# Kernel tuning notes

Measured on AMD Instinct MI355X. Metric: run time of the kernel, lower is better.

The kernel has to match this reference:

```python
import jax, jax.numpy as jnp
import numpy as np

D_MODEL = 1024
NUM_HEADS = 16
D_K = D_MODEL // NUM_HEADS


def setup_inputs() -> dict:
    key = jax.random.key(0)
    ks = jax.random.split(key, 5)
    s = 1.0 / np.sqrt(D_MODEL)  # xavier-ish scale
    x = jax.random.normal(ks[0], (2, 2048, D_MODEL), dtype=jnp.float32)
    Wq = jax.random.normal(ks[1], (D_MODEL, D_MODEL), dtype=jnp.float32) * s
    Wk = jax.random.normal(ks[2], (D_MODEL, D_MODEL), dtype=jnp.float32) * s
    Wv = jax.random.normal(ks[3], (D_MODEL, D_MODEL), dtype=jnp.float32) * s
    Wo = jax.random.normal(ks[4], (D_MODEL, D_MODEL), dtype=jnp.float32) * s
    z = jnp.zeros((D_MODEL,), dtype=jnp.float32)
    return {"x": x, "Wq": Wq, "bq": z, "Wk": Wk, "bk": z, "Wv": Wv, "bv": z, "Wo": Wo, "bo": z}


def reference(x, Wq, bq, Wk, bk, Wv, bv, Wo, bo):
    B, S, _ = x.shape
    # torch Linear: y = x @ W.T + b
    def split_heads(t):
        return t.reshape(B, S, NUM_HEADS, D_K).transpose(0, 2, 1, 3)  # [B,H,S,Dk]
    q = split_heads(x @ Wq.T + bq)
    k = split_heads(x @ Wk.T + bk)
    v = split_heads(x @ Wv.T + bv)
    scores = jnp.einsum('bhqd,bhkd->bhqk', q, k) / jnp.sqrt(jnp.float32(D_K))
    attn = jax.nn.softmax(scores, axis=-1)
    out = jnp.einsum('bhqk,bhkd->bhqd', attn, v)  # [B,H,S,Dk]
    out = out.transpose(0, 2, 1, 3).reshape(B, S, D_MODEL)
    return out @ Wo.T + bo
```

## Files before the change

### kernel.cpp

```cpp
#include <hip/hip_runtime.h>
#include <hip/hip_bf16.h>
#include <type_traits>


typedef __attribute__((ext_vector_type(4))) float f32x4;
typedef __attribute__((ext_vector_type(16))) float f32x16;
typedef __attribute__((ext_vector_type(8))) short s16x8;
typedef __attribute__((ext_vector_type(4))) unsigned int u32x4;

#define GLDS16(g, l)                                                       \
  __builtin_amdgcn_global_load_lds(                                        \
      (const __attribute__((address_space(1))) unsigned int*)(g),          \
      (__attribute__((address_space(3))) unsigned int*)(l), 16, 0, 0)

#define SCALE_Q 0.18033688011112042f

__device__ __forceinline__ unsigned short f2bf(float f) {
  unsigned int u = __builtin_bit_cast(unsigned int, f);
  u += 0x7fffu + ((u >> 16) & 1u);
  return (unsigned short)(u >> 16);
}

__device__ __forceinline__ unsigned int cvtpk_bf16(float lo, float hi) {
  unsigned int r;
  asm("v_cvt_pk_bf16_f32 %0, %1, %2" : "=v"(r) : "v"(lo), "v"(hi));
  return r;
}

__device__ __forceinline__ float fexp2(float x) {
  return __builtin_amdgcn_exp2f(x);
}

__global__ void cvt_all(const float* __restrict__ x, const float* __restrict__ Wq,
                        const float* __restrict__ Wk, const float* __restrict__ Wv,
                        const float* __restrict__ Wo, const float* __restrict__ bq,
                        const float* __restrict__ bk, const float* __restrict__ bv,
                        unsigned short* __restrict__ xb,
                        unsigned short* __restrict__ wcat,
                        unsigned short* __restrict__ wob,
                        float* __restrict__ bcat) {
  int g = blockIdx.x * blockDim.x + threadIdx.x;
  if (g >= 2097152) {
    int off = (g - 2097152) * 4;
    const float* src;
    float sc = 1.0f;
    int o2 = off;
    if (off < 1024) {
      src = bq; sc = SCALE_Q;
    } else if (off < 2048) {
      src = bk; o2 = off - 1024;
    } else {
      src = bv; o2 = off - 2048;
    }
    float4 v = *reinterpret_cast<const float4*>(src + o2);
    float4 w;
    w.x = v.x * sc; w.y = v.y * sc; w.z = v.z * sc; w.w = v.w * sc;
    *reinterpret_cast<float4*>(bcat + off) = w;
    return;
  }
  const float* in;
  unsigned short* out;
  int off;
  float scale = 1.0f;
  if (g < 1048576) {
    in = x; out = xb; off = g;
  } else if (g < 1310720) {
    in = Wq; out = wcat; off = g - 1048576; scale = SCALE_Q;
  } else if (g < 1572864) {
    in = Wk; out = wcat + 1048576; off = g - 1310720;
  } else if (g < 1835008) {
    in = Wv; out = wcat + 2097152; off = g - 1572864;
  } else {
    in = Wo; out = wob; off = g - 1835008;
  }
  float4 v = *reinterpret_cast<const float4*>(in + off * 4);
  ushort4 o;
  o.x = f2bf(v.x * scale); o.y = f2bf(v.y * scale);
  o.z = f2bf(v.z * scale); o.w = f2bf(v.w * scale);
  *reinterpret_cast<ushort4*>(out + off * 4) = o;
}

__global__ __launch_bounds__(256, 3) void gemm_qkv(
    const unsigned short* __restrict__ A, const unsigned short* __restrict__ B,
    unsigned short* __restrict__ C, unsigned short* __restrict__ vtp,
    const float* __restrict__ bias) {
  __shared__ __align__(16) unsigned short As[3 * 128 * 32];
  __shared__ __align__(16) unsigned short Bs[3 * 128 * 32];

  const int tid = threadIdx.x;
  const int lane = tid & 63, wv = tid >> 6;
  const int g = lane >> 4, c16 = lane & 15;
  const int wm = wv >> 1, wn = wv & 1;
  const int bn = blockIdx.x, bm = blockIdx.y;

  const unsigned short* Ab = A + (size_t)(bm * 128) * 1024;
  const unsigned short* Bb = B + (size_t)(bn * 128) * 1024;

  const int r0 = tid >> 2, cc0 = (tid & 3) * 8;
  const int r1 = r0 + 64;
  const int cs0 = cc0 ^ ((r0 & 8) << 1);
  const int cs1 = cc0 ^ ((r1 & 8) << 1);
  const int rc = (g * 8) ^ ((c16 & 8) << 1);

  f32x4 acc[4][4] = {};

#define STG(mat, base, kt, slot)                                           \
  {                                                                        \
    GLDS16(base + (size_t)r0 * 1024 + (kt) * 32 + cs0,                     \
           mat + (slot) * 4096 + r0 * 32 + cc0);                           \
    GLDS16(base + (size_t)r1 * 1024 + (kt) * 32 + cs1,                     \
           mat + (slot) * 4096 + r1 * 32 + cc0);                           \
  }

  STG(As, Ab, 0, 0)
  STG(Bs, Bb, 0, 0)
  STG(As, Ab, 1, 1)
  STG(Bs, Bb, 1, 1)

  int slot = 0, slot2 = 2;
  for (int t = 0; t < 32; ++t) {
    if (t < 31) {
      asm volatile("s_waitcnt vmcnt(4)" ::: "memory");
    } else {
      asm volatile("s_waitcnt vmcnt(0)" ::: "memory");
    }
    __builtin_amdgcn_s_barrier();
    if (t < 30) {
      STG(As, Ab, t + 2, slot2)
      STG(Bs, Bb, t + 2, slot2)
    }
    s16x8 af[4], bf[4];
#pragma unroll
    for (int mf = 0; mf < 4; ++mf)
      af[mf] = *(const s16x8*)&As[slot * 4096 +
                                  (wm * 64 + mf * 16 + c16) * 32 + rc];
#pragma unroll
    for (int nf = 0; nf < 4; ++nf)
      bf[nf] = *(const s16x8*)&Bs[slot * 4096 +
                                  (wn * 64 + nf * 16 + c16) * 32 + rc];
    __builtin_amdgcn_s_setprio(1);
#pragma unroll
    for (int mf = 0; mf < 4; ++mf)
#pragma unroll
      for (int nf = 0; nf < 4; ++nf)
        acc[mf][nf] = __builtin_amdgcn_mfma_f32_16x16x32_bf16(
            af[mf], bf[nf], acc[mf][nf], 0, 0, 0);
    __builtin_amdgcn_s_setprio(0);
    slot = (slot == 2) ? 0 : slot + 1;
    slot2 = (slot2 == 2) ? 0 : slot2 + 1;
  }
#undef STG

#pragma unroll
  for (int mf = 0; mf < 4; ++mf) {
#pragma unroll
    for (int nf = 0; nf < 4; ++nf) {
      int col = bn * 128 + wn * 64 + nf * 16 + c16;
      float bb = bias[col];
      int row0 = bm * 128 + wm * 64 + mf * 16 + g * 4;
      if (col >= 2048) {
        int d = col - 2048, hh = d >> 6, dl = d & 63;
        int b_ = row0 >> 11, s = row0 & 2047;
        ushort4 pk;
        pk.x = f2bf(acc[mf][nf][0] + bb);
        pk.y = f2bf(acc[mf][nf][1] + bb);
        pk.z = f2bf(acc[mf][nf][2] + bb);
        pk.w = f2bf(acc[mf][nf][3] + bb);
        *reinterpret_cast<ushort4*>(
            vtp + ((size_t)((b_ * 16 + hh) * 64 + dl)) * 2048 + s) = pk;
      } else {
#pragma unroll
        for (int j = 0; j < 4; ++j)
          C[(size_t)(row0 + j) * 3072 + col] = f2bf(acc[mf][nf][j] + bb);
      }
    }
  }
}

__global__ __launch_bounds__(256, 4) void gemm_out64(
    const unsigned short* __restrict__ A, const unsigned short* __restrict__ B,
    float* __restrict__ C, const float* __restrict__ bias) {
  __shared__ __align__(16) unsigned short As[3 * 128 * 32];
  __shared__ __align__(16) unsigned short Bs[3 * 64 * 32];

  const int tid = threadIdx.x;
  const int lane = tid & 63, wv = tid >> 6;
  const int g = lane >> 4, c16 = lane & 15;
  const int wm = wv >> 1, wn = wv & 1;
  const int bn = blockIdx.x, bm = blockIdx.y;

  const unsigned short* Ab = A + (size_t)(bm * 128) * 1024;
  const unsigned short* Bb = B + (size_t)(bn * 64) * 1024;

  const int r0 = tid >> 2, cc0 = (tid & 3) * 8;
  const int r1 = r0 + 64;
  const int cs0 = cc0 ^ ((r0 & 8) << 1);
  const int cs1 = cc0 ^ ((r1 & 8) << 1);
  const int rc = (g * 8) ^ ((c16 & 8) << 1);

  f32x4 acc[4][2] = {};

#define STG64(kt, slot)                                                    \
  {                                                                        \
    GLDS16(Ab + (size_t)r0 * 1024 + (kt) * 32 + cs0,                       \
           As + (slot) * 4096 + r0 * 32 + cc0);                            \
    GLDS16(Ab + (size_t)r1 * 1024 + (kt) * 32 + cs1,                       \
           As + (slot) * 4096 + r1 * 32 + cc0);                            \
    GLDS16(Bb + (size_t)r0 * 1024 + (kt) * 32 + cs0,                       \
           Bs + (slot) * 2048 + r0 * 32 + cc0);                            \
  }

  STG64(0, 0)
  STG64(1, 1)

  int slot = 0, slot2 = 2;
  for (int t = 0; t < 32; ++t) {
    if (t < 31) {
      asm volatile("s_waitcnt vmcnt(3)" ::: "memory");
    } else {
      asm volatile("s_waitcnt vmcnt(0)" ::: "memory");
    }
    __builtin_amdgcn_s_barrier();
    if (t < 30) STG64(t + 2, slot2)
    s16x8 af[4], bf[2];
#pragma unroll
    for (int mf = 0; mf < 4; ++mf)
      af[mf] = *(const s16x8*)&As[slot * 4096 +
                                  (wm * 64 + mf * 16 + c16) * 32 + rc];
#pragma unroll
    for (int nf = 0; nf < 2; ++nf)
      bf[nf] = *(const s16x8*)&Bs[slot * 2048 +
                                  (wn * 32 + nf * 16 + c16) * 32 + rc];
    __builtin_amdgcn_s_setprio(1);
#pragma unroll
    for (int mf = 0; mf < 4; ++mf)
#pragma unroll
      for (int nf = 0; nf < 2; ++nf)
        acc[mf][nf] = __builtin_amdgcn_mfma_f32_16x16x32_bf16(
            af[mf], bf[nf], acc[mf][nf], 0, 0, 0);
    __builtin_amdgcn_s_setprio(0);
    slot = (slot == 2) ? 0 : slot + 1;
    slot2 = (slot2 == 2) ? 0 : slot2 + 1;
  }
#undef STG64

#pragma unroll
  for (int mf = 0; mf < 4; ++mf) {
#pragma unroll
    for (int nf = 0; nf < 2; ++nf) {
      int col = bn * 64 + wn * 32 + nf * 16 + c16;
      float bb = bias[col];
      int row0 = bm * 128 + wm * 64 + mf * 16 + g * 4;
#pragma unroll
      for (int j = 0; j < 4; ++j)
        C[(size_t)(row0 + j) * 1024 + col] = acc[mf][nf][j] + bb;
    }
  }
}

__global__ __launch_bounds__(1024) void flash_attn(
    const unsigned short* __restrict__ qkv, const unsigned short* __restrict__ vt,
    unsigned short* __restrict__ attn) {
  __shared__ __align__(16) char smem[131072];
  unsigned short* KsB = (unsigned short*)smem;
  unsigned short* VTsB = (unsigned short*)(smem + 65536);
  float* MoB = (float*)smem;
  float* MlB = (float*)(smem + 66560);

  const int tid = threadIdx.x;
  const int wv = tid >> 6, lane = tid & 63;
  const int half = wv >> 3, w8 = wv & 7;
  const int col = lane & 31, hi = lane >> 5;
  const int bh = blockIdx.x, qt = blockIdx.y;
  const int b = bh >> 4, h = bh & 15;
  const int qrow0 = qt * 256 + w8 * 32;

  const int stid = tid & 511;
  const int srow = stid >> 3, scs = stid & 7;
  const int sqc = ((scs - (srow >> 3)) & 7) ^ (srow & 7);
  const int kbase = half * 1024;
  const unsigned short* kgsrc =
      qkv + (size_t)(b * 2048 + kbase + srow) * 3072 + 1024 + h * 64 + sqc * 8;
  const unsigned short* vgsrc =
      vt + (size_t)(bh * 64 + srow) * 2048 + kbase + sqc * 8;

  s16x8 qb[4];
#pragma unroll
  for (int ds = 0; ds < 4; ++ds)
    qb[ds] = *(const s16x8*)(qkv + (size_t)(b * 2048 + qrow0 + col) * 3072 +
                             h * 64 + ds * 16 + hi * 8);

  s16x8 onev;
#pragma unroll
  for (int j = 0; j < 8; ++j) onev[j] = (short)0x3F80;

  f32x16 o[2] = {};
  f32x16 lacc = {};

  GLDS16(kgsrc, &KsB[(half * 4 + 0) * 4096 + stid * 8]);
  GLDS16(vgsrc, &VTsB[(half * 4 + 0) * 4096 + stid * 8]);
  GLDS16(kgsrc + (size_t)64 * 3072, &KsB[(half * 4 + 1) * 4096 + stid * 8]);
  GLDS16(vgsrc + 64, &VTsB[(half * 4 + 1) * 4096 + stid * 8]);

  for (int kt = 0; kt < 16; ++kt) {
    const int buf = kt & 3;
    const unsigned short* Kc = &KsB[(half * 4 + buf) * 4096];
    const unsigned short* Vc = &VTsB[(half * 4 + buf) * 4096];
    if (kt < 14) {
      const int nb = (kt + 2) & 3;
      GLDS16(kgsrc + (size_t)(kt + 2) * 64 * 3072,
             &KsB[(half * 4 + nb) * 4096 + stid * 8]);
      GLDS16(vgsrc + (kt + 2) * 64, &VTsB[(half * 4 + nb) * 4096 + stid * 8]);
      asm volatile("s_waitcnt vmcnt(4)" ::: "memory");
    } else if (kt == 14) {
      asm volatile("s_waitcnt vmcnt(2)" ::: "memory");
    } else {
      asm volatile("s_waitcnt vmcnt(0)" ::: "memory");
    }
    __builtin_amdgcn_s_barrier();

    f32x16 st[2];
    __builtin_amdgcn_s_setprio(1);
#pragma unroll
    for (int kb = 0; kb < 2; ++kb) {
      f32x16 a = {};
#pragma unroll
      for (int ds = 0; ds < 4; ++ds) {
        int row = kb * 32 + col;
        int cs = ds * 2 + hi;
        int hoff = ((cs ^ (row & 7)) + (row >> 3)) & 7;
        s16x8 ka = *(const s16x8*)&Kc[row * 64 + hoff * 8];
        a = __builtin_amdgcn_mfma_f32_32x32x16_bf16(ka, qb[ds], a, 0, 0, 0);
      }
      st[kb] = a;
    }
    __builtin_amdgcn_s_setprio(0);

#pragma unroll
    for (int kb = 0; kb < 2; ++kb)
#pragma unroll
      for (int r = 0; r < 16; ++r) st[kb][r] = fexp2(st[kb][r]);

#pragma unroll
    for (int kb = 0; kb < 2; ++kb) {
#pragma unroll
      for (int hf = 0; hf < 2; ++hf) {
        const int p0 = hf * 8;
        unsigned int a0 = cvtpk_bf16(st[kb][p0 + 0], st[kb][p0 + 1]);
        unsigned int b0 = cvtpk_bf16(st[kb][p0 + 4], st[kb][p0 + 5]);
        unsigned int a1 = cvtpk_bf16(st[kb][p0 + 2], st[kb][p0 + 3]);
        unsigned int b1 = cvtpk_bf16(st[kb][p0 + 6], st[kb][p0 + 7]);
        asm("v_permlane32_swap_b32 %0, %1" : "+v"(a0), "+v"(b0));
        asm("v_permlane32_swap_b32 %0, %1" : "+v"(a1), "+v"(b1));
        u32x4 pw;
        pw[0] = a0; pw[1] = a1; pw[2] = b0; pw[3] = b1;
        const s16x8 pa = __builtin_bit_cast(s16x8, pw);
        const int ks = kb * 2 + hf;
        __builtin_amdgcn_s_setprio(1);
#pragma unroll
        for (int n = 0; n < 2; ++n) {
          int row = n * 32 + col;
          int cs = ks * 2 + hi;
          int hoff = ((cs ^ (row & 7)) + (row >> 3)) & 7;
          s16x8 vb = *(const s16x8*)&Vc[row * 64 + hoff * 8];
          o[n] = __builtin_amdgcn_mfma_f32_32x32x16_bf16(pa, vb, o[n], 0, 0, 0);
        }
        lacc = __builtin_amdgcn_mfma_f32_32x32x16_bf16(pa, onev, lacc, 0, 0, 0);
        __builtin_amdgcn_s_setprio(0);
      }
    }
  }
  __syncthreads();

  if (half == 1) {
#pragma unroll
    for (int r = 0; r < 16; ++r) {
      int qd = (r & 3) + 8 * (r >> 2) + 4 * hi;
      MoB[(w8 * 32 + qd) * 65 + col] = o[0][r];
      MoB[(w8 * 32 + qd) * 65 + 32 + col] = o[1][r];
      if (col == 0) MlB[w8 * 32 + qd] = lacc[r];
    }
  }
  __syncthreads();
  if (half == 0) {
#pragma unroll
    for (int r = 0; r < 16; ++r) {
      int qd = (r & 3) + 8 * (r >> 2) + 4 * hi;
      float linv = 1.f / (lacc[r] + MlB[w8 * 32 + qd]);
      float v0 = (o[0][r] + MoB[(w8 * 32 + qd) * 65 + col]) * linv;
      float v1 = (o[1][r] + MoB[(w8 * 32 + qd) * 65 + 32 + col]) * linv;
      size_t base = (size_t)(b * 2048 + qrow0 + qd) * 1024 + h * 64;
      attn[base + col] = f2bf(v0);
      attn[base + 32 + col] = f2bf(v1);
    }
  }
}

extern "C" void kernel_launch(void* const* d_in, const int* in_sizes, int n_in,
                              void* d_out, int out_size, void* d_ws, size_t ws_size,
                              hipStream_t stream) {
  const float* x  = (const float*)d_in[0];
  const float* Wq = (const float*)d_in[1];
  const float* bq = (const float*)d_in[2];
  const float* Wk = (const float*)d_in[3];
  const float* bk = (const float*)d_in[4];
  const float* Wv = (const float*)d_in[5];
  const float* bv = (const float*)d_in[6];
  const float* Wo = (const float*)d_in[7];
  const float* bo = (const float*)d_in[8];
  float* out = (float*)d_out;

  char* ws = (char*)d_ws;
  const size_t MB = 1024 * 1024;
  unsigned short* xb   = (unsigned short*)(ws + 0);
  unsigned short* attn = (unsigned short*)(ws + 0);
  unsigned short* wob  = (unsigned short*)(ws + 8 * MB);
  unsigned short* wcat = (unsigned short*)(ws + 10 * MB);
  unsigned short* qkv  = (unsigned short*)(ws + 18 * MB);
  unsigned short* vt   = (unsigned short*)(ws + 42 * MB);
  float* bcat          = (float*)(ws + 50 * MB);

  cvt_all<<<8195, 256, 0, stream>>>(x, Wq, Wk, Wv, Wo, bq, bk, bv, xb, wcat,
                                    wob, bcat);

  gemm_qkv<<<dim3(24, 32), 256, 0, stream>>>(xb, wcat, qkv, vt, bcat);

  flash_attn<<<dim3(32, 8), 1024, 0, stream>>>(qkv, vt, attn);

  gemm_out64<<<dim3(16, 32), 256, 0, stream>>>(attn, wob, out, bo);
}
```

Baseline: 108.4 us.

## Process two 32-row query groups per wave in flash attention, halving block threads

```diff
diff --git a/kernel.cpp b/kernel.cpp
--- a/kernel.cpp
+++ b/kernel.cpp
@@ -258,7 +258,7 @@
   }
 }
 
-__global__ __launch_bounds__(1024) void flash_attn(
+__global__ __launch_bounds__(512) void flash_attn(
     const unsigned short* __restrict__ qkv, const unsigned short* __restrict__ vt,
     unsigned short* __restrict__ attn) {
   __shared__ __align__(16) char smem[131072];
@@ -269,92 +269,114 @@
 
   const int tid = threadIdx.x;
   const int wv = tid >> 6, lane = tid & 63;
-  const int half = wv >> 3, w8 = wv & 7;
+  const int half = wv >> 2, w4 = wv & 3;
   const int col = lane & 31, hi = lane >> 5;
   const int bh = blockIdx.x, qt = blockIdx.y;
   const int b = bh >> 4, h = bh & 15;
-  const int qrow0 = qt * 256 + w8 * 32;
-
-  const int stid = tid & 511;
-  const int srow = stid >> 3, scs = stid & 7;
-  const int sqc = ((scs - (srow >> 3)) & 7) ^ (srow & 7);
+  const int qrow0 = qt * 256 + w4 * 64;
+
+  const int stid = tid & 255;
+  const int idx0 = stid, idx1 = stid + 256;
+  const int sr0 = idx0 >> 3, sq0 = (((idx0 & 7) - (sr0 >> 3)) & 7) ^ (sr0 & 7);
+  const int sr1 = idx1 >> 3, sq1 = (((idx1 & 7) - (sr1 >> 3)) & 7) ^ (sr1 & 7);
   const int kbase = half * 1024;
-  const unsigned short* kgsrc =
-      qkv + (size_t)(b * 2048 + kbase + srow) * 3072 + 1024 + h * 64 + sqc * 8;
-  const unsigned short* vgsrc =
-      vt + (size_t)(bh * 64 + srow) * 2048 + kbase + sqc * 8;
-
-  s16x8 qb[4];
-#pragma unroll
-  for (int ds = 0; ds < 4; ++ds)
-    qb[ds] = *(const s16x8*)(qkv + (size_t)(b * 2048 + qrow0 + col) * 3072 +
-                             h * 64 + ds * 16 + hi * 8);
+  const unsigned short* kg0 =
+      qkv + (size_t)(b * 2048 + kbase + sr0) * 3072 + 1024 + h * 64 + sq0 * 8;
+  const unsigned short* kg1 =
+      qkv + (size_t)(b * 2048 + kbase + sr1) * 3072 + 1024 + h * 64 + sq1 * 8;
+  const unsigned short* vg0 =
+      vt + (size_t)(bh * 64 + sr0) * 2048 + kbase + sq0 * 8;
+  const unsigned short* vg1 =
+      vt + (size_t)(bh * 64 + sr1) * 2048 + kbase + sq1 * 8;
+
+#define STGF(kt, bf)                                                       \
+  {                                                                        \
+    unsigned short* kd = &KsB[(half * 4 + (bf)) * 4096];                   \
+    unsigned short* vd = &VTsB[(half * 4 + (bf)) * 4096];                  \
+    const size_t ko = (size_t)(kt) * 64 * 3072;                            \
+    GLDS16(kg0 + ko, &kd[idx0 * 8]);                                       \
+    GLDS16(kg1 + ko, &kd[idx1 * 8]);                                       \
+    GLDS16(vg0 + (kt) * 64, &vd[idx0 * 8]);                                \
+    GLDS16(vg1 + (kt) * 64, &vd[idx1 * 8]);                                \
+  }
+
+  s16x8 qb[2][4];
+#pragma unroll
+  for (int g2 = 0; g2 < 2; ++g2)
+#pragma unroll
+    for (int ds = 0; ds < 4; ++ds)
+      qb[g2][ds] = *(const s16x8*)(qkv +
+                                   (size_t)(b * 2048 + qrow0 + g2 * 32 + col) *
+                                       3072 +
+                                   h * 64 + ds * 16 + hi * 8);
 
   s16x8 onev;
 #pragma unroll
   for (int j = 0; j < 8; ++j) onev[j] = (short)0x3F80;
 
-  f32x16 o[2] = {};
-  f32x16 lacc = {};
-
-  GLDS16(kgsrc, &KsB[(half * 4 + 0) * 4096 + stid * 8]);
-  GLDS16(vgsrc, &VTsB[(half * 4 + 0) * 4096 + stid * 8]);
-  GLDS16(kgsrc + (size_t)64 * 3072, &KsB[(half * 4 + 1) * 4096 + stid * 8]);
-  GLDS16(vgsrc + 64, &VTsB[(half * 4 + 1) * 4096 + stid * 8]);
+  f32x16 o[2][2] = {};
+  f32x16 lacc[2] = {};
+
+  STGF(0, 0)
+  STGF(1, 1)
 
   for (int kt = 0; kt < 16; ++kt) {
     const int buf = kt & 3;
     const unsigned short* Kc = &KsB[(half * 4 + buf) * 4096];
     const unsigned short* Vc = &VTsB[(half * 4 + buf) * 4096];
     if (kt < 14) {
-      const int nb = (kt + 2) & 3;
-      GLDS16(kgsrc + (size_t)(kt + 2) * 64 * 3072,
-             &KsB[(half * 4 + nb) * 4096 + stid * 8]);
-      GLDS16(vgsrc + (kt + 2) * 64, &VTsB[(half * 4 + nb) * 4096 + stid * 8]);
+      STGF(kt + 2, (kt + 2) & 3)
+      asm volatile("s_waitcnt vmcnt(8)" ::: "memory");
+    } else if (kt == 14) {
       asm volatile("s_waitcnt vmcnt(4)" ::: "memory");
-    } else if (kt == 14) {
-      asm volatile("s_waitcnt vmcnt(2)" ::: "memory");
     } else {
       asm volatile("s_waitcnt vmcnt(0)" ::: "memory");
     }
     __builtin_amdgcn_s_barrier();
 
-    f32x16 st[2];
+    f32x16 st[2][2] = {};
     __builtin_amdgcn_s_setprio(1);
 #pragma unroll
     for (int kb = 0; kb < 2; ++kb) {
-      f32x16 a = {};
 #pragma unroll
       for (int ds = 0; ds < 4; ++ds) {
         int row = kb * 32 + col;
         int cs = ds * 2 + hi;
         int hoff = ((cs ^ (row & 7)) + (row >> 3)) & 7;
         s16x8 ka = *(const s16x8*)&Kc[row * 64 + hoff * 8];
-        a = __builtin_amdgcn_mfma_f32_32x32x16_bf16(ka, qb[ds], a, 0, 0, 0);
+        st[0][kb] = __builtin_amdgcn_mfma_f32_32x32x16_bf16(ka, qb[0][ds],
+                                                            st[0][kb], 0, 0, 0);
+        st[1][kb] = __builtin_amdgcn_mfma_f32_32x32x16_bf16(ka, qb[1][ds],
+                                                            st[1][kb], 0, 0, 0);
       }
-      st[kb] = a;
     }
     __builtin_amdgcn_s_setprio(0);
 
 #pragma unroll
-    for (int kb = 0; kb < 2; ++kb)
-#pragma unroll
-      for (int r = 0; r < 16; ++r) st[kb][r] = fexp2(st[kb][r]);
+    for (int g2 = 0; g2 < 2; ++g2)
+#pragma unroll
+      for (int kb = 0; kb < 2; ++kb)
+#pragma unroll
+        for (int r = 0; r < 16; ++r) st[g2][kb][r] = fexp2(st[g2][kb][r]);
 
 #pragma unroll
     for (int kb = 0; kb < 2; ++kb) {
 #pragma unroll
       for (int hf = 0; hf < 2; ++hf) {
         const int p0 = hf * 8;
-        unsigned int a0 = cvtpk_bf16(st[kb][p0 + 0], st[kb][p0 + 1]);
-        unsigned int b0 = cvtpk_bf16(st[kb][p0 + 4], st[kb][p0 + 5]);
-        unsigned int a1 = cvtpk_bf16(st[kb][p0 + 2], st[kb][p0 + 3]);
-        unsigned int b1 = cvtpk_bf16(st[kb][p0 + 6], st[kb][p0 + 7]);
-        asm("v_permlane32_swap_b32 %0, %1" : "+v"(a0), "+v"(b0));
-        asm("v_permlane32_swap_b32 %0, %1" : "+v"(a1), "+v"(b1));
-        u32x4 pw;
-        pw[0] = a0; pw[1] = a1; pw[2] = b0; pw[3] = b1;
-        const s16x8 pa = __builtin_bit_cast(s16x8, pw);
+        s16x8 pa[2];
+#pragma unroll
+        for (int g2 = 0; g2 < 2; ++g2) {
+          unsigned int a0 = cvtpk_bf16(st[g2][kb][p0 + 0], st[g2][kb][p0 + 1]);
+          unsigned int b0 = cvtpk_bf16(st[g2][kb][p0 + 4], st[g2][kb][p0 + 5]);
+          unsigned int a1 = cvtpk_bf16(st[g2][kb][p0 + 2], st[g2][kb][p0 + 3]);
+          unsigned int b1 = cvtpk_bf16(st[g2][kb][p0 + 6], st[g2][kb][p0 + 7]);
+          asm("v_permlane32_swap_b32 %0, %1" : "+v"(a0), "+v"(b0));
+          asm("v_permlane32_swap_b32 %0, %1" : "+v"(a1), "+v"(b1));
+          u32x4 pw;
+          pw[0] = a0; pw[1] = a1; pw[2] = b0; pw[3] = b1;
+          pa[g2] = __builtin_bit_cast(s16x8, pw);
+        }
         const int ks = kb * 2 + hf;
         __builtin_amdgcn_s_setprio(1);
 #pragma unroll
@@ -363,35 +385,50 @@
           int cs = ks * 2 + hi;
           int hoff = ((cs ^ (row & 7)) + (row >> 3)) & 7;
           s16x8 vb = *(const s16x8*)&Vc[row * 64 + hoff * 8];
-          o[n] = __builtin_amdgcn_mfma_f32_32x32x16_bf16(pa, vb, o[n], 0, 0, 0);
+          o[0][n] = __builtin_amdgcn_mfma_f32_32x32x16_bf16(pa[0], vb, o[0][n],
+                                                            0, 0, 0);
+          o[1][n] = __builtin_amdgcn_mfma_f32_32x32x16_bf16(pa[1], vb, o[1][n],
+                                                            0, 0, 0);
         }
-        lacc = __builtin_amdgcn_mfma_f32_32x32x16_bf16(pa, onev, lacc, 0, 0, 0);
+        lacc[0] =
+            __builtin_amdgcn_mfma_f32_32x32x16_bf16(pa[0], onev, lacc[0], 0, 0, 0);
+        lacc[1] =
+            __builtin_amdgcn_mfma_f32_32x32x16_bf16(pa[1], onev, lacc[1], 0, 0, 0);
         __builtin_amdgcn_s_setprio(0);
       }
     }
   }
+#undef STGF
   __syncthreads();
 
   if (half == 1) {
 #pragma unroll
-    for (int r = 0; r < 16; ++r) {
-      int qd = (r & 3) + 8 * (r >> 2) + 4 * hi;
-      MoB[(w8 * 32 + qd) * 65 + col] = o[0][r];
-      MoB[(w8 * 32 + qd) * 65 + 32 + col] = o[1][r];
-      if (col == 0) MlB[w8 * 32 + qd] = lacc[r];
+    for (int g2 = 0; g2 < 2; ++g2) {
+#pragma unroll
+      for (int r = 0; r < 16; ++r) {
+        int qd = (r & 3) + 8 * (r >> 2) + 4 * hi;
+        int row = w4 * 64 + g2 * 32 + qd;
+        MoB[row * 65 + col] = o[g2][0][r];
+        MoB[row * 65 + 32 + col] = o[g2][1][r];
+        if (col == 0) MlB[row] = lacc[g2][r];
+      }
     }
   }
   __syncthreads();
   if (half == 0) {
 #pragma unroll
-    for (int r = 0; r < 16; ++r) {
-      int qd = (r & 3) + 8 * (r >> 2) + 4 * hi;
-      float linv = 1.f / (lacc[r] + MlB[w8 * 32 + qd]);
-      float v0 = (o[0][r] + MoB[(w8 * 32 + qd) * 65 + col]) * linv;
-      float v1 = (o[1][r] + MoB[(w8 * 32 + qd) * 65 + 32 + col]) * linv;
-      size_t base = (size_t)(b * 2048 + qrow0 + qd) * 1024 + h * 64;
-      attn[base + col] = f2bf(v0);
-      attn[base + 32 + col] = f2bf(v1);
+    for (int g2 = 0; g2 < 2; ++g2) {
+#pragma unroll
+      for (int r = 0; r < 16; ++r) {
+        int qd = (r & 3) + 8 * (r >> 2) + 4 * hi;
+        int row = w4 * 64 + g2 * 32 + qd;
+        float linv = 1.f / (lacc[g2][r] + MlB[row]);
+        float v0 = (o[g2][0][r] + MoB[row * 65 + col]) * linv;
+        float v1 = (o[g2][1][r] + MoB[row * 65 + 32 + col]) * linv;
+        size_t base = (size_t)(b * 2048 + qt * 256 + row) * 1024 + h * 64;
+        attn[base + col] = f2bf(v0);
+        attn[base + 32 + col] = f2bf(v1);
+      }
     }
   }
 }
@@ -425,7 +462,7 @@
 
   gemm_qkv<<<dim3(24, 32), 256, 0, stream>>>(xb, wcat, qkv, vt, bcat);
 
-  flash_attn<<<dim3(32, 8), 1024, 0, stream>>>(qkv, vt, attn);
+  flash_attn<<<dim3(32, 8), 512, 0, stream>>>(qkv, vt, attn);
 
   gemm_out64<<<dim3(16, 32), 256, 0, stream>>>(attn, wob, out, bo);
 }
```

After: 109.0 us. About the same (+0.5%).

## Shrink attention K/V pipeline to double buffering and simplify LDS swizzle

Applied to the files above, without the earlier changes.

```diff
diff --git a/kernel.cpp b/kernel.cpp
--- a/kernel.cpp
+++ b/kernel.cpp
@@ -261,9 +261,9 @@
 __global__ __launch_bounds__(1024) void flash_attn(
     const unsigned short* __restrict__ qkv, const unsigned short* __restrict__ vt,
     unsigned short* __restrict__ attn) {
-  __shared__ __align__(16) char smem[131072];
+  __shared__ __align__(16) char smem[68608];
   unsigned short* KsB = (unsigned short*)smem;
-  unsigned short* VTsB = (unsigned short*)(smem + 65536);
+  unsigned short* VTsB = (unsigned short*)(smem + 32768);
   float* MoB = (float*)smem;
   float* MlB = (float*)(smem + 66560);
 
@@ -271,13 +271,13 @@
   const int wv = tid >> 6, lane = tid & 63;
   const int half = wv >> 3, w8 = wv & 7;
   const int col = lane & 31, hi = lane >> 5;
-  const int bh = blockIdx.x, qt = blockIdx.y;
+  const int qt = blockIdx.x, bh = blockIdx.y;
   const int b = bh >> 4, h = bh & 15;
   const int qrow0 = qt * 256 + w8 * 32;
 
   const int stid = tid & 511;
   const int srow = stid >> 3, scs = stid & 7;
-  const int sqc = ((scs - (srow >> 3)) & 7) ^ (srow & 7);
+  const int sqc = scs ^ (srow & 7);
   const int kbase = half * 1024;
   const unsigned short* kgsrc =
       qkv + (size_t)(b * 2048 + kbase + srow) * 3072 + 1024 + h * 64 + sqc * 8;
@@ -297,27 +297,20 @@
   f32x16 o[2] = {};
   f32x16 lacc = {};
 
-  GLDS16(kgsrc, &KsB[(half * 4 + 0) * 4096 + stid * 8]);
-  GLDS16(vgsrc, &VTsB[(half * 4 + 0) * 4096 + stid * 8]);
-  GLDS16(kgsrc + (size_t)64 * 3072, &KsB[(half * 4 + 1) * 4096 + stid * 8]);
-  GLDS16(vgsrc + 64, &VTsB[(half * 4 + 1) * 4096 + stid * 8]);
+  GLDS16(kgsrc, &KsB[half * 8192 + stid * 8]);
+  GLDS16(vgsrc, &VTsB[half * 8192 + stid * 8]);
+  __syncthreads();
 
   for (int kt = 0; kt < 16; ++kt) {
-    const int buf = kt & 3;
-    const unsigned short* Kc = &KsB[(half * 4 + buf) * 4096];
-    const unsigned short* Vc = &VTsB[(half * 4 + buf) * 4096];
-    if (kt < 14) {
-      const int nb = (kt + 2) & 3;
-      GLDS16(kgsrc + (size_t)(kt + 2) * 64 * 3072,
-             &KsB[(half * 4 + nb) * 4096 + stid * 8]);
-      GLDS16(vgsrc + (kt + 2) * 64, &VTsB[(half * 4 + nb) * 4096 + stid * 8]);
-      asm volatile("s_waitcnt vmcnt(4)" ::: "memory");
-    } else if (kt == 14) {
-      asm volatile("s_waitcnt vmcnt(2)" ::: "memory");
-    } else {
-      asm volatile("s_waitcnt vmcnt(0)" ::: "memory");
-    }
-    __builtin_amdgcn_s_barrier();
+    const int cur = kt & 1;
+    const unsigned short* Kc = &KsB[(half * 2 + cur) * 4096];
+    const unsigned short* Vc = &VTsB[(half * 2 + cur) * 4096];
+    if (kt < 15) {
+      GLDS16(kgsrc + (size_t)(kt + 1) * 64 * 3072,
+             &KsB[(half * 2 + (cur ^ 1)) * 4096 + stid * 8]);
+      GLDS16(vgsrc + (kt + 1) * 64,
+             &VTsB[(half * 2 + (cur ^ 1)) * 4096 + stid * 8]);
+    }
 
     f32x16 st[2];
     __builtin_amdgcn_s_setprio(1);
@@ -328,8 +321,7 @@
       for (int ds = 0; ds < 4; ++ds) {
         int row = kb * 32 + col;
         int cs = ds * 2 + hi;
-        int hoff = ((cs ^ (row & 7)) + (row >> 3)) & 7;
-        s16x8 ka = *(const s16x8*)&Kc[row * 64 + hoff * 8];
+        s16x8 ka = *(const s16x8*)&Kc[row * 64 + (cs ^ (row & 7)) * 8];
         a = __builtin_amdgcn_mfma_f32_32x32x16_bf16(ka, qb[ds], a, 0, 0, 0);
       }
       st[kb] = a;
@@ -361,16 +353,15 @@
         for (int n = 0; n < 2; ++n) {
           int row = n * 32 + col;
           int cs = ks * 2 + hi;
-          int hoff = ((cs ^ (row & 7)) + (row >> 3)) & 7;
-          s16x8 vb = *(const s16x8*)&Vc[row * 64 + hoff * 8];
+          s16x8 vb = *(const s16x8*)&Vc[row * 64 + (cs ^ (row & 7)) * 8];
           o[n] = __builtin_amdgcn_mfma_f32_32x32x16_bf16(pa, vb, o[n], 0, 0, 0);
         }
         lacc = __builtin_amdgcn_mfma_f32_32x32x16_bf16(pa, onev, lacc, 0, 0, 0);
         __builtin_amdgcn_s_setprio(0);
       }
     }
-  }
-  __syncthreads();
+    __syncthreads();
+  }
 
   if (half == 1) {
 #pragma unroll
@@ -425,7 +416,7 @@
 
   gemm_qkv<<<dim3(24, 32), 256, 0, stream>>>(xb, wcat, qkv, vt, bcat);
 
-  flash_attn<<<dim3(32, 8), 1024, 0, stream>>>(qkv, vt, attn);
+  flash_attn<<<dim3(8, 32), 1024, 0, stream>>>(qkv, vt, attn);
 
   gemm_out64<<<dim3(16, 32), 256, 0, stream>>>(attn, wob, out, bo);
 }
```

Measured after the change: 107.4 us. No clear change (-0.9%).
